# Kernel optimization log

Hardware: AMD Instinct MI355X
Metric: run time of the kernel (lower is better)

The kernel has to match this reference:

```python
import jax, jax.numpy as jnp
import numpy as np

K = 2  # top-k routing (init kwarg k=2)


def setup_inputs() -> dict:
    key = jax.random.key(0)
    k1, k2 = jax.random.split(key)
    in_flow = jax.random.normal(k1, (8192, 2048), dtype=jnp.float32)
    gates = jax.random.uniform(k2, (8192, 8), dtype=jnp.float32)
    return {"in_flow": in_flow, "gates": gates}


def reference(in_flow, gates):
    # in_flow: [N, D] tokens; gates: [N, E]
    N, E = gates.shape
    # --- gen_indices (topk branch): one-hot-k routing mask [N, E] ---
    top_idx = jax.lax.top_k(gates, K)[1]                       # [N, K]
    mask = jnp.zeros((N, E), dtype=jnp.int32)
    mask = mask.at[jnp.arange(N)[:, None], top_idx].set(1)     # scatter_(1, idx, 1)
    # --- dispatch: per-expert gather, concatenated expert-major ---
    # torch.nonzero(mask.T[i]) returns token indices ascending per expert;
    # stable argsort of expert-major flattened mask reproduces exactly that
    # concatenation order, and topk guarantees exactly N*K selected rows.
    flat = mask.T.reshape(-1)                                  # [E*N], expert-major
    order = jnp.argsort(-flat)                                 # stable: ones first, in order
    sel = order[: N * K]                                       # flat positions of assignments
    token_idx = sel % N                                        # [N*K] source token per row
    out_data = in_flow[token_idx]                              # [N*K, D] routed flow
    out_tags = token_idx                                       # tags (pack_invalid_flow arange tags)
    counts = mask.sum(axis=0)                                  # [E] rows per destination (loads)
    return out_data, out_tags, counts
```

## Files before the change

kernel.cpp:

```cpp
#include <hip/hip_runtime.h>
#include <hip/hip_bf16.h>


#define EXPERTS 8
#define TOPK 2
#define BLK 256

__global__ void k_mask_count(const float* __restrict__ gates,
                             int* __restrict__ masks,
                             int* __restrict__ block_counts) {
    int n = blockIdx.x * BLK + threadIdx.x;
    const float4* g4 = (const float4*)(gates + (size_t)n * EXPERTS);
    float4 a = g4[0], b = g4[1];
    float v[EXPERTS] = {a.x, a.y, a.z, a.w, b.x, b.y, b.z, b.w};

    int e1 = 0; float b1 = v[0];
    #pragma unroll
    for (int e = 1; e < EXPERTS; e++) if (v[e] > b1) { b1 = v[e]; e1 = e; }
    int e2 = -1; float b2 = -1e30f;
    #pragma unroll
    for (int e = 0; e < EXPERTS; e++) if (e != e1 && v[e] > b2) { b2 = v[e]; e2 = e; }

    int mask = (1 << e1) | (1 << e2);
    masks[n] = mask;

    int wave = threadIdx.x >> 6;
    int lane = threadIdx.x & 63;
    __shared__ int wc[BLK / 64][EXPERTS];
    #pragma unroll
    for (int e = 0; e < EXPERTS; e++) {
        unsigned long long bal = __ballot((mask >> e) & 1);
        if (lane == 0) wc[wave][e] = __popcll(bal);
    }
    __syncthreads();
    if (threadIdx.x < EXPERTS) {
        int e = threadIdx.x;
        int t = 0;
        #pragma unroll
        for (int w = 0; w < BLK / 64; w++) t += wc[w][e];
        block_counts[blockIdx.x * EXPERTS + e] = t;
    }
}

__global__ void k_scan(const int* __restrict__ block_counts,
                       int* __restrict__ block_offsets,
                       float* __restrict__ counts_out, int NB) {
    __shared__ int tot[EXPERTS];
    __shared__ int base[EXPERTS];
    int e = threadIdx.x;
    if (e < EXPERTS) {
        int t = 0;
        for (int b = 0; b < NB; b++) t += block_counts[b * EXPERTS + e];
        tot[e] = t;
        counts_out[e] = (float)t;
    }
    __syncthreads();
    if (threadIdx.x == 0) {
        int acc = 0;
        for (int i = 0; i < EXPERTS; i++) { base[i] = acc; acc += tot[i]; }
    }
    __syncthreads();
    if (e < EXPERTS) {
        int acc = base[e];
        for (int b = 0; b < NB; b++) {
            block_offsets[b * EXPERTS + e] = acc;
            acc += block_counts[b * EXPERTS + e];
        }
    }
}

__global__ void k_pos(const int* __restrict__ masks,
                      const int* __restrict__ block_offsets,
                      int* __restrict__ tok_of_pos) {
    int n = blockIdx.x * BLK + threadIdx.x;
    int mask = masks[n];
    int wave = threadIdx.x >> 6;
    int lane = threadIdx.x & 63;
    __shared__ int wc[BLK / 64][EXPERTS];
    unsigned long long bal[EXPERTS];
    #pragma unroll
    for (int e = 0; e < EXPERTS; e++) {
        bal[e] = __ballot((mask >> e) & 1);
        if (lane == 0) wc[wave][e] = __popcll(bal[e]);
    }
    __syncthreads();
    unsigned long long below = (lane == 0) ? 0ull : ((~0ull) >> (64 - lane));
    #pragma unroll
    for (int e = 0; e < EXPERTS; e++) {
        if ((mask >> e) & 1) {
            int wbase = 0;
            for (int w = 0; w < wave; w++) wbase += wc[w][e];
            int r = __popcll(bal[e] & below);
            int pos = block_offsets[blockIdx.x * EXPERTS + e] + wbase + r;
            tok_of_pos[pos] = n;
        }
    }
}

__global__ void k_copy(const float* __restrict__ in_flow,
                       const int* __restrict__ tok_of_pos,
                       float* __restrict__ out_data,
                       float* __restrict__ out_tags, int D) {
    int p = blockIdx.x;
    int tok = tok_of_pos[p];
    if (threadIdx.x == 0) out_tags[p] = (float)tok;
    const float4* src = (const float4*)(in_flow + (size_t)tok * D);
    float4* dst = (float4*)(out_data + (size_t)p * D);
    int nv = D >> 2;
    for (int i = threadIdx.x; i < nv; i += BLK) dst[i] = src[i];
}

extern "C" void kernel_launch(void* const* d_in, const int* in_sizes, int n_in,
                              void* d_out, int out_size, void* d_ws, size_t ws_size,
                              hipStream_t stream) {
    const float* in_flow = (const float*)d_in[0];
    const float* gates   = (const float*)d_in[1];

    const int N  = in_sizes[1] / EXPERTS;
    const int D  = in_sizes[0] / N;
    const int NB = (N + BLK - 1) / BLK;
    const int NK = N * TOPK;

    int* masks         = (int*)d_ws;
    int* block_counts  = masks + N;
    int* block_offsets = block_counts + NB * EXPERTS;
    int* tok_of_pos    = block_offsets + NB * EXPERTS;

    float* out_data  = (float*)d_out;
    float* out_tags  = out_data + (size_t)NK * D;
    float* counts_out = out_tags + NK;

    hipLaunchKernelGGL(k_mask_count, dim3(NB), dim3(BLK), 0, stream,
                       gates, masks, block_counts);
    hipLaunchKernelGGL(k_scan, dim3(1), dim3(64), 0, stream,
                       block_counts, block_offsets, counts_out, NB);
    hipLaunchKernelGGL(k_pos, dim3(NB), dim3(BLK), 0, stream,
                       masks, block_offsets, tok_of_pos);
    hipLaunchKernelGGL(k_copy, dim3(NK), dim3(BLK), 0, stream,
                       in_flow, tok_of_pos, out_data, out_tags, D);
}
```

Measured before the change: 197.8 us.

## Fuse routing into single-block kernel and use wave-per-row persistent copy

```diff
diff --git a/kernel.cpp b/kernel.cpp
--- a/kernel.cpp
+++ b/kernel.cpp
@@ -4,110 +4,131 @@
 
 #define EXPERTS 8
 #define TOPK 2
-#define BLK 256
+#define N_TOK 8192
+#define NK (N_TOK * TOPK)
+#define RT_THREADS 1024
+#define TOK_PER_THR (N_TOK / RT_THREADS)
+#define RT_WAVES (RT_THREADS / 64)
 
-__global__ void k_mask_count(const float* __restrict__ gates,
-                             int* __restrict__ masks,
-                             int* __restrict__ block_counts) {
-    int n = blockIdx.x * BLK + threadIdx.x;
-    const float4* g4 = (const float4*)(gates + (size_t)n * EXPERTS);
-    float4 a = g4[0], b = g4[1];
-    float v[EXPERTS] = {a.x, a.y, a.z, a.w, b.x, b.y, b.z, b.w};
+__global__ __launch_bounds__(RT_THREADS) void k_route(
+        const float* __restrict__ gates,
+        int* __restrict__ tok_of_pos,
+        float* __restrict__ out_tags,
+        float* __restrict__ counts_out) {
+    const int t    = threadIdx.x;
+    const int wave = t >> 6;
+    const int lane = t & 63;
 
-    int e1 = 0; float b1 = v[0];
+    int mask[TOK_PER_THR];
+    int cnt[EXPERTS];
     #pragma unroll
-    for (int e = 1; e < EXPERTS; e++) if (v[e] > b1) { b1 = v[e]; e1 = e; }
-    int e2 = -1; float b2 = -1e30f;
+    for (int e = 0; e < EXPERTS; e++) cnt[e] = 0;
+
+    const float4* g4 = (const float4*)gates;
     #pragma unroll
-    for (int e = 0; e < EXPERTS; e++) if (e != e1 && v[e] > b2) { b2 = v[e]; e2 = e; }
+    for (int k = 0; k < TOK_PER_THR; k++) {
+        int n = t * TOK_PER_THR + k;
+        float4 a = g4[2 * n], b = g4[2 * n + 1];
+        float v[EXPERTS] = {a.x, a.y, a.z, a.w, b.x, b.y, b.z, b.w};
+        int e1 = 0; float b1 = v[0];
+        #pragma unroll
+        for (int e = 1; e < EXPERTS; e++) if (v[e] > b1) { b1 = v[e]; e1 = e; }
+        int e2 = -1; float b2 = -1e30f;
+        #pragma unroll
+        for (int e = 0; e < EXPERTS; e++) if (e != e1 && v[e] > b2) { b2 = v[e]; e2 = e; }
+        mask[k] = (1 << e1) | (1 << e2);
+        cnt[e1]++; cnt[e2]++;
+    }
 
-    int mask = (1 << e1) | (1 << e2);
-    masks[n] = mask;
+    int pk[4], incl[4];
+    #pragma unroll
+    for (int j = 0; j < 4; j++) pk[j] = cnt[2 * j] | (cnt[2 * j + 1] << 16);
 
-    int wave = threadIdx.x >> 6;
-    int lane = threadIdx.x & 63;
-    __shared__ int wc[BLK / 64][EXPERTS];
     #pragma unroll
-    for (int e = 0; e < EXPERTS; e++) {
-        unsigned long long bal = __ballot((mask >> e) & 1);
-        if (lane == 0) wc[wave][e] = __popcll(bal);
+    for (int j = 0; j < 4; j++) incl[j] = pk[j];
+    #pragma unroll
+    for (int d = 1; d < 64; d <<= 1) {
+        #pragma unroll
+        for (int j = 0; j < 4; j++) {
+            int up = __shfl_up(incl[j], d, 64);
+            if (lane >= d) incl[j] += up;
+        }
+    }
+
+    __shared__ int wtot[RT_WAVES][4];
+    if (lane == 63) {
+        #pragma unroll
+        for (int j = 0; j < 4; j++) wtot[wave][j] = incl[j];
     }
     __syncthreads();
-    if (threadIdx.x < EXPERTS) {
-        int e = threadIdx.x;
-        int t = 0;
+    int wpref[4], tot[4];
+    #pragma unroll
+    for (int j = 0; j < 4; j++) { wpref[j] = 0; tot[j] = 0; }
+    for (int w = 0; w < RT_WAVES; w++) {
         #pragma unroll
-        for (int w = 0; w < BLK / 64; w++) t += wc[w][e];
-        block_counts[blockIdx.x * EXPERTS + e] = t;
+        for (int j = 0; j < 4; j++) {
+            int x = wtot[w][j];
+            if (w < wave) wpref[j] += x;
+            tot[j] += x;
+        }
     }
+
+    int tote[EXPERTS], base[EXPERTS];
+    #pragma unroll
+    for (int j = 0; j < 4; j++) {
+        tote[2 * j]     = tot[j] & 0xFFFF;
+        tote[2 * j + 1] = (tot[j] >> 16) & 0xFFFF;
+    }
+    int acc = 0;
+    #pragma unroll
+    for (int e = 0; e < EXPERTS; e++) { base[e] = acc; acc += tote[e]; }
+
+    int rank[EXPERTS];
+    #pragma unroll
+    for (int j = 0; j < 4; j++) {
+        int excl = incl[j] - pk[j];
+        rank[2 * j]     = base[2 * j]     + ((wpref[j] + excl) & 0xFFFF);
+        rank[2 * j + 1] = base[2 * j + 1] + (((wpref[j] + excl) >> 16) & 0xFFFF);
+    }
+
+    #pragma unroll
+    for (int k = 0; k < TOK_PER_THR; k++) {
+        int n = t * TOK_PER_THR + k;
+        int m = mask[k];
+        #pragma unroll
+        for (int e = 0; e < EXPERTS; e++) {
+            if ((m >> e) & 1) {
+                int pos = rank[e]++;
+                tok_of_pos[pos] = n;
+                out_tags[pos] = (float)n;
+            }
+        }
+    }
+
+    if (t < EXPERTS) counts_out[t] = (float)tote[t];
 }
 
-__global__ void k_scan(const int* __restrict__ block_counts,
-                       int* __restrict__ block_offsets,
-                       float* __restrict__ counts_out, int NB) {
-    __shared__ int tot[EXPERTS];
-    __shared__ int base[EXPERTS];
-    int e = threadIdx.x;
-    if (e < EXPERTS) {
-        int t = 0;
-        for (int b = 0; b < NB; b++) t += block_counts[b * EXPERTS + e];
-        tot[e] = t;
-        counts_out[e] = (float)t;
+#define CP_BLOCKS 2048
+#define CP_THREADS 256
+
+__global__ __launch_bounds__(CP_THREADS) void k_copy(
+        const float* __restrict__ in_flow,
+        const int* __restrict__ tok_of_pos,
+        float* __restrict__ out_data, int D) {
+    const int lane   = threadIdx.x & 63;
+    const int wid    = blockIdx.x * (CP_THREADS / 64) + (threadIdx.x >> 6);
+    const int nwaves = CP_BLOCKS * (CP_THREADS / 64);
+
+    for (int p = wid; p < NK; p += nwaves) {
+        int tok = tok_of_pos[p];
+        const float4* src = (const float4*)(in_flow + (size_t)tok * D);
+        float4*       dst = (float4*)(out_data + (size_t)p * D);
+        float4 r[8];
+        #pragma unroll
+        for (int i = 0; i < 8; i++) r[i] = src[lane + 64 * i];
+        #pragma unroll
+        for (int i = 0; i < 8; i++) dst[lane + 64 * i] = r[i];
     }
-    __syncthreads();
-    if (threadIdx.x == 0) {
-        int acc = 0;
-        for (int i = 0; i < EXPERTS; i++) { base[i] = acc; acc += tot[i]; }
-    }
-    __syncthreads();
-    if (e < EXPERTS) {
-        int acc = base[e];
-        for (int b = 0; b < NB; b++) {
-            block_offsets[b * EXPERTS + e] = acc;
-            acc += block_counts[b * EXPERTS + e];
-        }
-    }
-}
-
-__global__ void k_pos(const int* __restrict__ masks,
-                      const int* __restrict__ block_offsets,
-                      int* __restrict__ tok_of_pos) {
-    int n = blockIdx.x * BLK + threadIdx.x;
-    int mask = masks[n];
-    int wave = threadIdx.x >> 6;
-    int lane = threadIdx.x & 63;
-    __shared__ int wc[BLK / 64][EXPERTS];
-    unsigned long long bal[EXPERTS];
-    #pragma unroll
-    for (int e = 0; e < EXPERTS; e++) {
-        bal[e] = __ballot((mask >> e) & 1);
-        if (lane == 0) wc[wave][e] = __popcll(bal[e]);
-    }
-    __syncthreads();
-    unsigned long long below = (lane == 0) ? 0ull : ((~0ull) >> (64 - lane));
-    #pragma unroll
-    for (int e = 0; e < EXPERTS; e++) {
-        if ((mask >> e) & 1) {
-            int wbase = 0;
-            for (int w = 0; w < wave; w++) wbase += wc[w][e];
-            int r = __popcll(bal[e] & below);
-            int pos = block_offsets[blockIdx.x * EXPERTS + e] + wbase + r;
-            tok_of_pos[pos] = n;
-        }
-    }
-}
-
-__global__ void k_copy(const float* __restrict__ in_flow,
-                       const int* __restrict__ tok_of_pos,
-                       float* __restrict__ out_data,
-                       float* __restrict__ out_tags, int D) {
-    int p = blockIdx.x;
-    int tok = tok_of_pos[p];
-    if (threadIdx.x == 0) out_tags[p] = (float)tok;
-    const float4* src = (const float4*)(in_flow + (size_t)tok * D);
-    float4* dst = (float4*)(out_data + (size_t)p * D);
-    int nv = D >> 2;
-    for (int i = threadIdx.x; i < nv; i += BLK) dst[i] = src[i];
 }
 
 extern "C" void kernel_launch(void* const* d_in, const int* in_sizes, int n_in,
@@ -115,27 +136,16 @@
                               hipStream_t stream) {
     const float* in_flow = (const float*)d_in[0];
     const float* gates   = (const float*)d_in[1];
+    const int D = in_sizes[0] / N_TOK;
 
-    const int N  = in_sizes[1] / EXPERTS;
-    const int D  = in_sizes[0] / N;
-    const int NB = (N + BLK - 1) / BLK;
-    const int NK = N * TOPK;
+    int* tok_of_pos = (int*)d_ws;
 
-    int* masks         = (int*)d_ws;
-    int* block_counts  = masks + N;
-    int* block_offsets = block_counts + NB * EXPERTS;
-    int* tok_of_pos    = block_offsets + NB * EXPERTS;
-
-    float* out_data  = (float*)d_out;
-    float* out_tags  = out_data + (size_t)NK * D;
+    float* out_data   = (float*)d_out;
+    float* out_tags   = out_data + (size_t)NK * D;
     float* counts_out = out_tags + NK;
 
-    hipLaunchKernelGGL(k_mask_count, dim3(NB), dim3(BLK), 0, stream,
-                       gates, masks, block_counts);
-    hipLaunchKernelGGL(k_scan, dim3(1), dim3(64), 0, stream,
-                       block_counts, block_offsets, counts_out, NB);
-    hipLaunchKernelGGL(k_pos, dim3(NB), dim3(BLK), 0, stream,
-                       masks, block_offsets, tok_of_pos);
-    hipLaunchKernelGGL(k_copy, dim3(NK), dim3(BLK), 0, stream,
-                       in_flow, tok_of_pos, out_data, out_tags, D);
+    hipLaunchKernelGGL(k_route, dim3(1), dim3(RT_THREADS), 0, stream,
+                       gates, tok_of_pos, out_tags, counts_out);
+    hipLaunchKernelGGL(k_copy, dim3(CP_BLOCKS), dim3(CP_THREADS), 0, stream,
+                       in_flow, tok_of_pos, out_data, D);
 }
```

Result: slower. 209.7 us (+6.0%).
